# Optimization experiments

Measured on AMD Instinct MI355X. Metric: run time of the kernel, lower is better.

Reference implementation:

```python
import jax, jax.numpy as jnp
import numpy as np

NUM_HEADS = 32
HEAD_DIM = 128
NUM_KV_HEADS = 8
SCALE = HEAD_DIM ** -0.5
BS = 2
SEQ_LEN = 2048


def setup_inputs() -> dict:
    key = jax.random.key(0)
    kq, kk, kv = jax.random.split(key, 3)
    q = jax.random.normal(kq, (BS * SEQ_LEN, NUM_HEADS * HEAD_DIM), dtype=jnp.float32)
    k = jax.random.normal(kk, (BS * SEQ_LEN, NUM_KV_HEADS * HEAD_DIM), dtype=jnp.float32)
    v = jax.random.normal(kv, (BS * SEQ_LEN, NUM_KV_HEADS * HEAD_DIM), dtype=jnp.float32)
    return {"q": q, "k": k, "v": v, "bs": BS, "seq_len": SEQ_LEN}


def reference(q, k, v, bs, seq_len):
    # Training-path: causal GQA attention (F.scaled_dot_product_attention, is_causal=True)
    qh = q.reshape(bs, seq_len, NUM_HEADS, HEAD_DIM)        # [b, s, h, d]
    kh = k.reshape(bs, seq_len, NUM_KV_HEADS, HEAD_DIM)     # [b, s, hk, d]
    vh = v.reshape(bs, seq_len, NUM_KV_HEADS, HEAD_DIM)
    rep = NUM_HEADS // NUM_KV_HEADS
    kh = jnp.repeat(kh, rep, axis=2)                         # [b, s, h, d]
    vh = jnp.repeat(vh, rep, axis=2)
    # scores [b, h, q, k]
    scores = jnp.einsum("bqhd,bkhd->bhqk", qh, kh) * SCALE
    causal = jnp.tril(jnp.ones((seq_len, seq_len), dtype=bool))
    scores = jnp.where(causal[None, None], scores, jnp.finfo(scores.dtype).min)
    probs = jax.nn.softmax(scores, axis=-1)
    o = jnp.einsum("bhqk,bkhd->bqhd", probs, vh)             # [b, q, h, d]
    return o.reshape(bs * seq_len, NUM_HEADS * HEAD_DIM)
```

## Files before the change

kernel.cpp:

```cpp
#include <hip/hip_runtime.h>

#define NUM_HEADS 32
#define HEAD_DIM 128
#define NUM_KV_HEADS 8
#define SEQ 2048
#define BATCH 2
#define BQ 128

typedef __attribute__((ext_vector_type(8))) short bf16x8;
typedef __attribute__((ext_vector_type(16))) float f32x16;
typedef __attribute__((ext_vector_type(4))) unsigned u32x4;

__device__ __forceinline__ short f2bf(float f) {
    unsigned u = __float_as_uint(f);
    u += 0x7fffu + ((u >> 16) & 1u);
    return (short)(u >> 16);
}
__device__ __forceinline__ unsigned pack2r(float a, float b) {
    unsigned ua = __float_as_uint(a) + 0x8000u;
    unsigned ub = __float_as_uint(b) + 0x8000u;
    return __builtin_amdgcn_perm(ub, ua, 0x07060302);
}
__device__ __forceinline__ float fexp2(float x) { return __builtin_amdgcn_exp2f(x); }

__global__ __launch_bounds__(256)
void conv_kv(const float* __restrict__ kg, const float* __restrict__ vg,
             short* __restrict__ kb, short* __restrict__ vt) {
    const int bid = blockIdx.x, tid = threadIdx.x;
    __shared__ float T[32][132];
    if (bid < 1024) {
        const float SL = 0.08838834764831845f * 1.4426950408889634f;
        int kvt = bid & 63, hk = (bid >> 6) & 7, b = bid >> 9;
#pragma unroll
        for (int i = 0; i < 4; ++i) {
            int slot = i * 256 + tid, row = slot >> 5, col = (slot & 31) * 4;
            float4 v = *(const float4*)(kg + ((size_t)(b * SEQ + kvt * 32 + row) * NUM_KV_HEADS + hk)
                                              * HEAD_DIM + col);
            *(float4*)&T[row][col] = v;
        }
        __syncthreads();
        short* dst = kb + (size_t)(b * NUM_KV_HEADS + hk) * SEQ * HEAD_DIM;
#pragma unroll
        for (int cc = 0; cc < 2; ++cc) {
            int c = tid * 2 + cc;
            int s = c >> 6, lane = c & 63, l32 = lane & 31, half = lane >> 5;
            float4 t0 = *(const float4*)&T[l32][s * 16 + half * 8];
            float4 t1 = *(const float4*)&T[l32][s * 16 + half * 8 + 4];
            bf16x8 o = { f2bf(t0.x * SL), f2bf(t0.y * SL), f2bf(t0.z * SL), f2bf(t0.w * SL),
                         f2bf(t1.x * SL), f2bf(t1.y * SL), f2bf(t1.z * SL), f2bf(t1.w * SL) };
            *(bf16x8*)(dst + ((size_t)(kvt * 8 + s) * 64 + lane) * 8) = o;
        }
    } else {
        int bidx = bid - 1024;
        int kvc = bidx & 63, hk = (bidx >> 6) & 7, b = bidx >> 9;
#pragma unroll
        for (int i = 0; i < 4; ++i) {
            int slot = i * 256 + tid, row = slot >> 5, col = (slot & 31) * 4;
            float4 v = *(const float4*)(vg + ((size_t)(b * SEQ + kvc * 32 + row) * NUM_KV_HEADS + hk)
                                              * HEAD_DIM + col);
            *(float4*)&T[row][col] = v;
        }
        __syncthreads();
        short* dst = vt + (size_t)(b * NUM_KV_HEADS + hk) * SEQ * HEAD_DIM;
#pragma unroll
        for (int cc = 0; cc < 2; ++cc) {
            int c = tid * 2 + cc;
            int chunk = c >> 6;
            int lane = c & 63, l32 = lane & 31, half = lane >> 5;
            int dtile = chunk >> 1, kk = chunk & 1;
            bf16x8 o;
#pragma unroll
            for (int j = 0; j < 8; ++j) o[j] = f2bf(T[kk * 16 + half * 8 + j][dtile * 32 + l32]);
            *(bf16x8*)(dst + ((size_t)(kvc * 8 + chunk) * 64 + lane) * 8) = o;
        }
    }
}

__device__ __forceinline__ void sm_pack(f32x16& s4, float& rls, int half,
                                        bf16x8& pfa, bf16x8& pfb) {
#pragma unroll
    for (int r = 0; r < 16; ++r) s4[r] = fexp2(s4[r]);
    {
        float t0 = (s4[0] + s4[1]) + (s4[2] + s4[3]);
        float t1 = (s4[4] + s4[5]) + (s4[6] + s4[7]);
        float t2 = (s4[8] + s4[9]) + (s4[10] + s4[11]);
        float t3 = (s4[12] + s4[13]) + (s4[14] + s4[15]);
        rls += (t0 + t1) + (t2 + t3);
    }
    unsigned p0 = pack2r(s4[0],  s4[1]);
    unsigned p1 = pack2r(s4[2],  s4[3]);
    unsigned p2 = pack2r(s4[4],  s4[5]);
    unsigned p3 = pack2r(s4[6],  s4[7]);
    unsigned p4 = pack2r(s4[8],  s4[9]);
    unsigned p5 = pack2r(s4[10], s4[11]);
    unsigned p6 = pack2r(s4[12], s4[13]);
    unsigned p7 = pack2r(s4[14], s4[15]);
    unsigned a0 = p0, b0 = p2;
    asm volatile("v_permlane32_swap_b32 %0, %1" : "+v"(a0), "+v"(b0));
    unsigned a1 = p1, b1 = p3;
    asm volatile("v_permlane32_swap_b32 %0, %1" : "+v"(a1), "+v"(b1));
    unsigned a2 = p4, b2 = p6;
    asm volatile("v_permlane32_swap_b32 %0, %1" : "+v"(a2), "+v"(b2));
    unsigned a3 = p5, b3 = p7;
    asm volatile("v_permlane32_swap_b32 %0, %1" : "+v"(a3), "+v"(b3));
    u32x4 w0 = { a0, a1, b0, b1 };
    u32x4 w1 = { a2, a3, b2, b3 };
    pfa = __builtin_bit_cast(bf16x8, w0);
    pfb = __builtin_bit_cast(bf16x8, w1);
}

template<bool MASK>
__device__ __forceinline__ void kv_step(const short* __restrict__ Ks,
                                        const short* __restrict__ Vs,
                                        const bf16x8 (&qf)[8], f32x16 (&o)[4],
                                        float& rls, int l32, int half, int lane) {
    f32x16 s4a, s4b;
#pragma unroll
    for (int r = 0; r < 16; ++r) { s4a[r] = 0.f; s4b[r] = 0.f; }
    {
        bf16x8 kf[4];
#pragma unroll
        for (int s = 0; s < 4; ++s)
            kf[s] = *(const bf16x8*)(Ks + (s << 9) + lane * 8);
#pragma unroll
        for (int s = 0; s < 4; ++s)
            s4a = __builtin_amdgcn_mfma_f32_32x32x16_bf16(kf[s], qf[s], s4a, 0, 0, 0);
    }
    {
        bf16x8 kf[4];
#pragma unroll
        for (int s = 0; s < 4; ++s)
            kf[s] = *(const bf16x8*)(Ks + ((4 + s) << 9) + lane * 8);
#pragma unroll
        for (int s = 0; s < 4; ++s)
            s4b = __builtin_amdgcn_mfma_f32_32x32x16_bf16(kf[s], qf[4 + s], s4b, 0, 0, 0);
    }
    f32x16 s4;
#pragma unroll
    for (int r = 0; r < 16; ++r) s4[r] = s4a[r] + s4b[r];

    if (MASK) {
#pragma unroll
        for (int r = 0; r < 16; ++r) {
            int klocal = (r & 3) + 8 * (r >> 2) + 4 * half;
            s4[r] = (klocal <= l32) ? s4[r] : -1e30f;
        }
    }

    bf16x8 pf0, pf1;
    sm_pack(s4, rls, half, pf0, pf1);

#pragma unroll
    for (int h2 = 0; h2 < 2; ++h2) {
        bf16x8 vf[4];
#pragma unroll
        for (int c = 0; c < 4; ++c)
            vf[c] = *(const bf16x8*)(Vs + ((h2 * 4 + c) << 9) + lane * 8);
#pragma unroll
        for (int c = 0; c < 4; ++c) {
            int cg = h2 * 4 + c;
            o[cg >> 1] = __builtin_amdgcn_mfma_f32_32x32x16_bf16(
                vf[c], (cg & 1) ? pf1 : pf0, o[cg >> 1], 0, 0, 0);
        }
    }
}

__global__ __launch_bounds__(256, 3)
void fattn_kernel(const float* __restrict__ qg, const short* __restrict__ kb,
                  const short* __restrict__ vt, float* __restrict__ outg) {
    __shared__ short sh[2][8192];

    const int tid  = threadIdx.x;
    const int wave = tid >> 6;
    const int lane = tid & 63;
    const int l32  = lane & 31;
    const int half = lane >> 5;

    const int bid  = (int)blockIdx.x;
    const int hk   = bid & 7;
    const int rest = bid >> 3;
    const int b    = rest & 1;
    const int hj   = (rest >> 1) & 3;
    const int qt   = 15 - (rest >> 3);
    const int h    = hk * 4 + hj;

    const int q0w = qt * BQ + wave * 32;

    bf16x8 qf[8];
    {
        const float* qp = qg + (size_t)(b * SEQ + q0w + l32) * (NUM_HEADS * HEAD_DIM)
                             + h * HEAD_DIM + half * 8;
#pragma unroll
        for (int s = 0; s < 8; ++s) {
            float4 a = *(const float4*)(qp + s * 16);
            float4 c = *(const float4*)(qp + s * 16 + 4);
            bf16x8 f = { f2bf(a.x), f2bf(a.y), f2bf(a.z), f2bf(a.w),
                         f2bf(c.x), f2bf(c.y), f2bf(c.z), f2bf(c.w) };
            qf[s] = f;
        }
    }

    const short* kreg = kb + (size_t)(b * NUM_KV_HEADS + hk) * SEQ * HEAD_DIM;
    const short* vreg = vt + (size_t)(b * NUM_KV_HEADS + hk) * SEQ * HEAD_DIM;

    f32x16 o[4];
#pragma unroll
    for (int dt = 0; dt < 4; ++dt)
#pragma unroll
        for (int r = 0; r < 16; ++r) o[dt][r] = 0.f;
    float rls = 0.f;

    const int nblk = 4 * qt + 4;
    const int nfw  = 4 * qt + wave;

#define STAGE(ktn, bf_)                                                           \
    {                                                                             \
        const short* ksrc_ = kreg + ((size_t)(ktn) << 12) + lane * 8;             \
        const short* vsrc_ = vreg + ((size_t)(ktn) << 12) + lane * 8;             \
        _Pragma("unroll")                                                         \
        for (int i_ = 0; i_ < 4; ++i_) {                                          \
            int ch_ = wave * 4 + i_;                                              \
            const short* g_ = (ch_ < 8) ? (ksrc_ + (ch_ << 9))                    \
                                        : (vsrc_ + ((ch_ - 8) << 9));             \
            __builtin_amdgcn_global_load_lds(                                     \
                (const __attribute__((address_space(1))) void*)g_,                \
                (__attribute__((address_space(3))) void*)&sh[bf_][ch_ << 9],      \
                16, 0, 0);                                                        \
        }                                                                         \
    }

    STAGE(0, 0);
    __syncthreads();

    int cur = 0;
    for (int kt = 0; kt < nblk; ++kt) {
        if (kt + 1 < nblk) STAGE(kt + 1, cur ^ 1);
        if (kt < nfw)
            kv_step<false>(&sh[cur][0], &sh[cur][4096], qf, o, rls, l32, half, lane);
        else if (kt == nfw)
            kv_step<true>(&sh[cur][0], &sh[cur][4096], qf, o, rls, l32, half, lane);
        __syncthreads();
        cur ^= 1;
    }
#undef STAGE

    const float rl = rls + __shfl_xor(rls, 32);
    const float inv = 1.0f / rl;

    float* op = outg + (size_t)(b * SEQ + q0w + l32) * (NUM_HEADS * HEAD_DIM) + h * HEAD_DIM;
#pragma unroll
    for (int dt = 0; dt < 4; ++dt)
#pragma unroll
        for (int blk = 0; blk < 4; ++blk) {
            float4 w = { o[dt][4 * blk + 0] * inv, o[dt][4 * blk + 1] * inv,
                         o[dt][4 * blk + 2] * inv, o[dt][4 * blk + 3] * inv };
            *(float4*)(op + dt * 32 + blk * 8 + half * 4) = w;
        }
}

extern "C" void kernel_launch(void* const* d_in, const int* in_sizes, int n_in,
                              void* d_out, int out_size, void* d_ws, size_t ws_size,
                              hipStream_t stream) {
    const float* q = (const float*)d_in[0];
    const float* k = (const float*)d_in[1];
    const float* v = (const float*)d_in[2];
    float* out = (float*)d_out;

    short* kbuf  = (short*)d_ws;
    short* vtbuf = kbuf + (size_t)BATCH * NUM_KV_HEADS * SEQ * HEAD_DIM;

    conv_kv<<<2048, 256, 0, stream>>>(k, v, kbuf, vtbuf);
    fattn_kernel<<<dim3(1024), dim3(256), 0, stream>>>(q, kbuf, vtbuf, out);
}
```

Baseline: 220.9 us.

## Triple-buffer KV staging with vmcnt waits, setprio around MFMAs, hardware bf16 pack

Moves K/V staging from double to triple buffering, prefetching two tiles ahead. Each iteration now has one explicit s_waitcnt vmcnt plus barrier instead of two __syncthreads, which lets global-to-LDS loads overlap more compute. It also wraps the MFMA groups in s_setprio, merges the two QK accumulators into one chain, and swaps the manual bf16 packing for v_cvt_pk_bf16_f32. The costs are more LDS per block, which may reduce occupancy, and a serial dependency chain of 8 MFMAs on one accumulator.

```diff
diff --git a/kernel.cpp b/kernel.cpp
--- a/kernel.cpp
+++ b/kernel.cpp
@@ -16,12 +16,12 @@
     u += 0x7fffu + ((u >> 16) & 1u);
     return (short)(u >> 16);
 }
-__device__ __forceinline__ unsigned pack2r(float a, float b) {
-    unsigned ua = __float_as_uint(a) + 0x8000u;
-    unsigned ub = __float_as_uint(b) + 0x8000u;
-    return __builtin_amdgcn_perm(ub, ua, 0x07060302);
-}
 __device__ __forceinline__ float fexp2(float x) { return __builtin_amdgcn_exp2f(x); }
+__device__ __forceinline__ unsigned cvtpk(float a, float b) {
+    unsigned r;
+    asm("v_cvt_pk_bf16_f32 %0, %1, %2" : "=v"(r) : "v"(a), "v"(b));
+    return r;
+}
 
 __global__ __launch_bounds__(256)
 void conv_kv(const float* __restrict__ kg, const float* __restrict__ vg,
@@ -87,14 +87,14 @@
         float t3 = (s4[12] + s4[13]) + (s4[14] + s4[15]);
         rls += (t0 + t1) + (t2 + t3);
     }
-    unsigned p0 = pack2r(s4[0],  s4[1]);
-    unsigned p1 = pack2r(s4[2],  s4[3]);
-    unsigned p2 = pack2r(s4[4],  s4[5]);
-    unsigned p3 = pack2r(s4[6],  s4[7]);
-    unsigned p4 = pack2r(s4[8],  s4[9]);
-    unsigned p5 = pack2r(s4[10], s4[11]);
-    unsigned p6 = pack2r(s4[12], s4[13]);
-    unsigned p7 = pack2r(s4[14], s4[15]);
+    unsigned p0 = cvtpk(s4[0],  s4[1]);
+    unsigned p1 = cvtpk(s4[2],  s4[3]);
+    unsigned p2 = cvtpk(s4[4],  s4[5]);
+    unsigned p3 = cvtpk(s4[6],  s4[7]);
+    unsigned p4 = cvtpk(s4[8],  s4[9]);
+    unsigned p5 = cvtpk(s4[10], s4[11]);
+    unsigned p6 = cvtpk(s4[12], s4[13]);
+    unsigned p7 = cvtpk(s4[14], s4[15]);
     unsigned a0 = p0, b0 = p2;
     asm volatile("v_permlane32_swap_b32 %0, %1" : "+v"(a0), "+v"(b0));
     unsigned a1 = p1, b1 = p3;
@@ -114,30 +114,21 @@
                                         const short* __restrict__ Vs,
                                         const bf16x8 (&qf)[8], f32x16 (&o)[4],
                                         float& rls, int l32, int half, int lane) {
-    f32x16 s4a, s4b;
-#pragma unroll
-    for (int r = 0; r < 16; ++r) { s4a[r] = 0.f; s4b[r] = 0.f; }
-    {
+    f32x16 s4;
+#pragma unroll
+    for (int r = 0; r < 16; ++r) s4[r] = 0.f;
+#pragma unroll
+    for (int h2 = 0; h2 < 2; ++h2) {
         bf16x8 kf[4];
 #pragma unroll
         for (int s = 0; s < 4; ++s)
-            kf[s] = *(const bf16x8*)(Ks + (s << 9) + lane * 8);
+            kf[s] = *(const bf16x8*)(Ks + ((h2 * 4 + s) << 9) + lane * 8);
+        __builtin_amdgcn_s_setprio(1);
 #pragma unroll
         for (int s = 0; s < 4; ++s)
-            s4a = __builtin_amdgcn_mfma_f32_32x32x16_bf16(kf[s], qf[s], s4a, 0, 0, 0);
-    }
-    {
-        bf16x8 kf[4];
-#pragma unroll
-        for (int s = 0; s < 4; ++s)
-            kf[s] = *(const bf16x8*)(Ks + ((4 + s) << 9) + lane * 8);
-#pragma unroll
-        for (int s = 0; s < 4; ++s)
-            s4b = __builtin_amdgcn_mfma_f32_32x32x16_bf16(kf[s], qf[4 + s], s4b, 0, 0, 0);
-    }
-    f32x16 s4;
-#pragma unroll
-    for (int r = 0; r < 16; ++r) s4[r] = s4a[r] + s4b[r];
+            s4 = __builtin_amdgcn_mfma_f32_32x32x16_bf16(kf[s], qf[h2 * 4 + s], s4, 0, 0, 0);
+        __builtin_amdgcn_s_setprio(0);
+    }
 
     if (MASK) {
 #pragma unroll
@@ -156,19 +147,21 @@
 #pragma unroll
         for (int c = 0; c < 4; ++c)
             vf[c] = *(const bf16x8*)(Vs + ((h2 * 4 + c) << 9) + lane * 8);
+        __builtin_amdgcn_s_setprio(1);
 #pragma unroll
         for (int c = 0; c < 4; ++c) {
             int cg = h2 * 4 + c;
             o[cg >> 1] = __builtin_amdgcn_mfma_f32_32x32x16_bf16(
                 vf[c], (cg & 1) ? pf1 : pf0, o[cg >> 1], 0, 0, 0);
         }
+        __builtin_amdgcn_s_setprio(0);
     }
 }
 
 __global__ __launch_bounds__(256, 3)
 void fattn_kernel(const float* __restrict__ qg, const short* __restrict__ kb,
                   const short* __restrict__ vt, float* __restrict__ outg) {
-    __shared__ short sh[2][8192];
+    __shared__ short sh[3][8192];
 
     const int tid  = threadIdx.x;
     const int wave = tid >> 6;
@@ -213,7 +206,7 @@
     const int nblk = 4 * qt + 4;
     const int nfw  = 4 * qt + wave;
 
-#define STAGE(ktn, bf_)                                                           \
+#define STAGE(ktn, p_)                                                            \
     {                                                                             \
         const short* ksrc_ = kreg + ((size_t)(ktn) << 12) + lane * 8;             \
         const short* vsrc_ = vreg + ((size_t)(ktn) << 12) + lane * 8;             \
@@ -224,23 +217,29 @@
                                         : (vsrc_ + ((ch_ - 8) << 9));             \
             __builtin_amdgcn_global_load_lds(                                     \
                 (const __attribute__((address_space(1))) void*)g_,                \
-                (__attribute__((address_space(3))) void*)&sh[bf_][ch_ << 9],      \
+                (__attribute__((address_space(3))) void*)((p_) + (ch_ << 9)),     \
                 16, 0, 0);                                                        \
         }                                                                         \
     }
 
-    STAGE(0, 0);
-    __syncthreads();
-
-    int cur = 0;
+    short* pA = &sh[0][0];
+    short* pB = &sh[1][0];
+    short* pC = &sh[2][0];
+
+    STAGE(0, pA);
+    STAGE(1, pB);
+
     for (int kt = 0; kt < nblk; ++kt) {
-        if (kt + 1 < nblk) STAGE(kt + 1, cur ^ 1);
+        if (kt < nblk - 1) asm volatile("s_waitcnt vmcnt(4)" ::: "memory");
+        else               asm volatile("s_waitcnt vmcnt(0)" ::: "memory");
+        __builtin_amdgcn_s_barrier();
+        __builtin_amdgcn_sched_barrier(0);
+        if (kt + 2 < nblk) STAGE(kt + 2, pC);
         if (kt < nfw)
-            kv_step<false>(&sh[cur][0], &sh[cur][4096], qf, o, rls, l32, half, lane);
+            kv_step<false>(pA, pA + 4096, qf, o, rls, l32, half, lane);
         else if (kt == nfw)
-            kv_step<true>(&sh[cur][0], &sh[cur][4096], qf, o, rls, l32, half, lane);
-        __syncthreads();
-        cur ^= 1;
+            kv_step<true>(pA, pA + 4096, qf, o, rls, l32, half, lane);
+        short* t = pA; pA = pB; pB = pC; pC = t;
     }
 #undef STAGE
 
```

Result: no change. 221.5 us (+0.3%).
